# Performance work log

Hardware: AMD Instinct MI355X
Metric: run time of the kernel (lower is better)

## Reference

```python
import jax, jax.numpy as jnp
import numpy as np

B, T, D, H = 4, 1024, 1024, 16
DH = D // H
BETA = 0.9


def setup_inputs() -> dict:
    key = jax.random.key(0)
    ks = jax.random.split(key, 9)
    s = 1.0 / np.sqrt(D)
    return {
        "x": jax.random.normal(ks[0], (B, T, D), jnp.float32),
        "l3_memory": jax.random.normal(ks[1], (B, 1, D), jnp.float32),
        "wq": jax.random.normal(ks[2], (D, D), jnp.float32) * s,
        "wk": jax.random.normal(ks[3], (D, D), jnp.float32) * s,
        "wv": jax.random.normal(ks[4], (D, D), jnp.float32) * s,
        "wo": jax.random.normal(ks[5], (D, D), jnp.float32) * s,
        "rw1": jax.random.normal(ks[6], (D, D // 2), jnp.float32) * s,
        "rb1": jnp.zeros((D // 2,), jnp.float32),
        "rw2": jax.random.normal(ks[7], (D // 2, 3), jnp.float32) * (1.0 / np.sqrt(D // 2)),
        "rb2": jnp.zeros((3,), jnp.float32),
    }


def reference(x, l3_memory, wq, wk, wv, wo, rw1, rb1, rw2, rb2):
    b, t, d = x.shape
    dh = d // H

    def heads(y):  # [b,t,d] -> [b,h,t,dh]
        return y.reshape(b, t, H, dh).transpose(0, 2, 1, 3)

    q = x @ wq
    qh = heads(q)

    # L2: causal prefix EMA along time: y_t = beta*y_{t-1} + (1-beta)*x_t, y_{-1}=0
    def ema_step(c, xt):
        y = BETA * c + (1.0 - BETA) * xt
        return y, y
    _, l2 = jax.lax.scan(ema_step, jnp.zeros((b, d), x.dtype), jnp.swapaxes(x, 0, 1))
    l2 = jnp.swapaxes(l2, 0, 1)

    # L3: retrieval memory repeated to sequence length
    l3 = jnp.broadcast_to(l3_memory, (b, t, d))

    mask = jnp.tril(jnp.ones((t, t), bool))
    neg = jnp.finfo(x.dtype).min
    scale = 1.0 / np.sqrt(dh)

    def attend(mem):
        kh = heads(mem @ wk)
        vh = heads(mem @ wv)
        s = jnp.einsum('bhqd,bhkd->bhqk', qh, kh) * scale
        s = jnp.where(mask[None, None], s, neg)
        p = jax.nn.softmax(s, axis=-1)
        return jnp.einsum('bhqk,bhkd->bhqd', p, vh)

    # router over q tokens -> softmax mixture weights [b,t,3]
    hdn = jax.nn.gelu(q @ rw1 + rb1, approximate=False)
    lam = jax.nn.softmax(hdn @ rw2 + rb2, axis=-1)

    mixed = jnp.zeros((b, H, t, dh), x.dtype)
    for i, mem in enumerate((x, l2, l3)):
        mixed = mixed + lam[:, None, :, i:i + 1] * attend(mem)

    out = mixed.transpose(0, 2, 1, 3).reshape(b, t, d) @ wo
    return out, lam
```

## Files before the change

kernel.cpp:

```cpp
#include <hip/hip_runtime.h>
#include <hip/hip_bf16.h>
#include <math.h>


#define B_ 4
#define T_ 1024
#define D_ 1024
#define H_ 16
#define DH_ 64
#define M_ 4096

#define ECH 64
#define NCH 16

typedef __attribute__((ext_vector_type(8))) short bf16x8;
typedef __attribute__((ext_vector_type(4))) short s16x4;
typedef __attribute__((ext_vector_type(4))) float f32x4;
typedef __attribute__((ext_vector_type(4))) unsigned int u32x4;

__device__ inline short f2b(float f) {
  __hip_bfloat16 h = __float2bfloat16(f);
  return *reinterpret_cast<short*>(&h);
}

__device__ inline unsigned int pack2(float lo, float hi) {
  return ((unsigned int)(unsigned short)f2b(hi) << 16) |
         (unsigned int)(unsigned short)f2b(lo);
}

__device__ inline void gload_lds16(const short* g, short* l) {
  __builtin_amdgcn_global_load_lds(
      (const __attribute__((address_space(1))) unsigned int*)g,
      (__attribute__((address_space(3))) unsigned int*)l, 16, 0, 0);
}

__global__ __launch_bounds__(256) void ema_chunk_kernel(const float* __restrict__ x,
                                                        float* __restrict__ l2,
                                                        short* __restrict__ xb) {
  int idx = blockIdx.x * 256 + threadIdx.x;
  int d = idx & (D_ - 1);
  int ch = (idx >> 10) & (NCH - 1);
  int b = idx >> 14;
  const float* xp = x + (size_t)(b * T_ + ch * ECH) * D_ + d;
  float* yp = l2 + (size_t)(b * T_ + ch * ECH) * D_ + d;
  short* xbp = xb + (size_t)(b * T_ + ch * ECH) * D_ + d;
  float y = 0.f;
#pragma unroll 4
  for (int t = 0; t < ECH; ++t) {
    float xv = xp[t * D_];
    y = 0.9f * y + 0.1f * xv;
    yp[t * D_] = y;
    xbp[t * D_] = f2b(xv);
  }
}

__global__ __launch_bounds__(256) void ema_carry_kernel(const float* __restrict__ l2,
                                                        float* __restrict__ g) {
  int idx = blockIdx.x * 256 + threadIdx.x;
  int d = idx & (D_ - 1);
  int b = idx >> 10;
  const float b64 = 0.0011790184577739f;
  float G = 0.f;
  for (int ch = 0; ch < NCH; ++ch) {
    g[(size_t)(b * NCH + ch) * D_ + d] = G;
    float lf = l2[(size_t)(b * T_ + ch * ECH + ECH - 1) * D_ + d];
    G = lf + b64 * G;
  }
}

__global__ __launch_bounds__(256) void ema_fix_kernel(const float* __restrict__ l2,
                                                      const float* __restrict__ g,
                                                      short* __restrict__ l2b) {
  int idx = blockIdx.x * 256 + threadIdx.x;
  int d = idx & (D_ - 1);
  int t = (idx >> 10) & (T_ - 1);
  int b = idx >> 20;
  int ch = t >> 6;
  int off = t & (ECH - 1);
  float G = g[(size_t)(b * NCH + ch) * D_ + d];
  float p9 = exp2f((float)(off + 1) * -0.15200309344504997f);
  l2b[idx] = f2b(l2[idx] + p9 * G);
}

__global__ __launch_bounds__(256) void transpose_w_kernel(
    const float* __restrict__ w0, const float* __restrict__ w1,
    const float* __restrict__ w2, const float* __restrict__ w3,
    const float* __restrict__ w4,
    short* __restrict__ t0, short* __restrict__ t1, short* __restrict__ t2,
    short* __restrict__ t3, short* __restrict__ t4) {
  int z = blockIdx.z;
  const float* W = (z == 0) ? w0 : (z == 1) ? w1 : (z == 2) ? w2 : (z == 3) ? w3 : w4;
  short* Wt = (z == 0) ? t0 : (z == 1) ? t1 : (z == 2) ? t2 : (z == 3) ? t3 : t4;
  int cols = (z == 4) ? 512 : 1024;
  int c0 = blockIdx.x * 32, r0 = blockIdx.y * 32;
  if (c0 >= cols) return;
  __shared__ float tile[32][33];
  int tc = threadIdx.x & 31, tr8 = threadIdx.x >> 5;
#pragma unroll
  for (int i = 0; i < 4; ++i)
    tile[tr8 + i * 8][tc] = W[(size_t)(r0 + tr8 + i * 8) * cols + c0 + tc];
  __syncthreads();
#pragma unroll
  for (int i = 0; i < 4; ++i) {
    int rr = tr8 + i * 8;
    Wt[(size_t)(c0 + rr) * 1024 + r0 + tc] = f2b(tile[tc][rr]);
  }
}

template <int NB>
__global__ __launch_bounds__(256) void gemm_bt(const short* __restrict__ A, int lda,
                                               const short* __restrict__ Bt,
                                               float* __restrict__ Cf,
                                               short* __restrict__ Cb,
                                               int Ndim, int Kdim) {
  __shared__ short As[128 * 64];
  __shared__ short Bs[NB * 64];
  constexpr int NW = NB / 64;
  constexpr int NF = 4;
  constexpr int MF = (NW == 2) ? 4 : 2;
  int tid = threadIdx.x;
  int w = tid >> 6, l = tid & 63;
  int lg = l >> 4, ll = l & 15;
  int wr = (NW == 2) ? (w >> 1) : w;
  int wc = (NW == 2) ? (w & 1) : 0;
  int row0 = blockIdx.y * 128, col0 = blockIdx.x * NB;

  f32x4 acc[MF][NF];
#pragma unroll
  for (int m = 0; m < MF; ++m)
#pragma unroll
    for (int n = 0; n < NF; ++n) acc[m][n] = (f32x4){0.f, 0.f, 0.f, 0.f};

  for (int k0 = 0; k0 < Kdim; k0 += 64) {
    __syncthreads();
#pragma unroll
    for (int it = 0; it < 4; ++it) {
      int s = it * 256 + w * 64 + l;
      int r = s >> 3;
      int c = (s & 7) ^ (r & 7);
      gload_lds16(A + (size_t)(row0 + r) * lda + k0 + c * 8, &As[(it * 256 + w * 64) * 8]);
    }
#pragma unroll
    for (int it = 0; it < NB / 32; ++it) {
      int s = it * 256 + w * 64 + l;
      int r = s >> 3;
      int c = (s & 7) ^ (r & 7);
      gload_lds16(Bt + (size_t)(col0 + r) * Kdim + k0 + c * 8, &Bs[(it * 256 + w * 64) * 8]);
    }
    __syncthreads();
#pragma unroll
    for (int ks = 0; ks < 2; ++ks) {
      bf16x8 af[MF], bfr[NF];
#pragma unroll
      for (int m = 0; m < MF; ++m) {
        int r = wr * (MF * 16) + m * 16 + ll;
        af[m] = *(const bf16x8*)&As[r * 64 + (((ks * 4 + lg) ^ (r & 7)) << 3)];
      }
#pragma unroll
      for (int n = 0; n < NF; ++n) {
        int r = wc * 64 + n * 16 + ll;
        bfr[n] = *(const bf16x8*)&Bs[r * 64 + (((ks * 4 + lg) ^ (r & 7)) << 3)];
      }
#pragma unroll
      for (int m = 0; m < MF; ++m)
#pragma unroll
        for (int n = 0; n < NF; ++n)
          acc[m][n] = __builtin_amdgcn_mfma_f32_16x16x32_bf16(af[m], bfr[n], acc[m][n], 0, 0, 0);
    }
  }
#pragma unroll
  for (int m = 0; m < MF; ++m) {
    int gr = row0 + wr * (MF * 16) + m * 16 + lg * 4;
#pragma unroll
    for (int n = 0; n < NF; ++n) {
      int gc = col0 + wc * 64 + n * 16 + ll;
#pragma unroll
      for (int r = 0; r < 4; ++r) {
        float vv = acc[m][n][r];
        if (Cf) Cf[(size_t)(gr + r) * Ndim + gc] = vv;
        if (Cb) Cb[(size_t)(gr + r) * Ndim + gc] = f2b(vv);
      }
    }
  }
}

__global__ __launch_bounds__(256) void gemm_dual(const short* __restrict__ xb,
                                                 const short* __restrict__ l2b,
                                                 const short* __restrict__ wqkvT,
                                                 short* __restrict__ QKV,
                                                 short* __restrict__ KV2) {
  int lin = blockIdx.y * 40 + blockIdx.x;
  int lin2 = (lin & 7) * 160 + (lin >> 3);
  int bx = lin2 % 40;
  int by = lin2 / 40;

  const short* A;
  const short* Bt;
  short* Cb;
  int Ndim, col0;
  if (bx < 24) {
    A = xb; Bt = wqkvT; Cb = QKV; Ndim = 3072; col0 = bx * 128;
  } else {
    A = l2b; Bt = wqkvT + 1024 * 1024; Cb = KV2; Ndim = 2048; col0 = (bx - 24) * 128;
  }
  __shared__ short As[128 * 64];
  __shared__ short Bs[128 * 64];
  int tid = threadIdx.x;
  int w = tid >> 6, l = tid & 63;
  int lg = l >> 4, ll = l & 15;
  int wr = w >> 1, wc = w & 1;
  int row0 = by * 128;

  f32x4 acc[4][4];
#pragma unroll
  for (int m = 0; m < 4; ++m)
#pragma unroll
    for (int n = 0; n < 4; ++n) acc[m][n] = (f32x4){0.f, 0.f, 0.f, 0.f};

  for (int k0 = 0; k0 < 1024; k0 += 64) {
    __syncthreads();
#pragma unroll
    for (int it = 0; it < 4; ++it) {
      int s = it * 256 + w * 64 + l;
      int r = s >> 3;
      int c = (s & 7) ^ (r & 7);
      gload_lds16(A + (size_t)(row0 + r) * 1024 + k0 + c * 8, &As[(it * 256 + w * 64) * 8]);
      gload_lds16(Bt + (size_t)(col0 + r) * 1024 + k0 + c * 8, &Bs[(it * 256 + w * 64) * 8]);
    }
    __syncthreads();
#pragma unroll
    for (int ks = 0; ks < 2; ++ks) {
      bf16x8 af[4], bfr[4];
#pragma unroll
      for (int m = 0; m < 4; ++m) {
        int r = wr * 64 + m * 16 + ll;
        af[m] = *(const bf16x8*)&As[r * 64 + (((ks * 4 + lg) ^ (r & 7)) << 3)];
      }
#pragma unroll
      for (int n = 0; n < 4; ++n) {
        int r = wc * 64 + n * 16 + ll;
        bfr[n] = *(const bf16x8*)&Bs[r * 64 + (((ks * 4 + lg) ^ (r & 7)) << 3)];
      }
#pragma unroll
      for (int m = 0; m < 4; ++m)
#pragma unroll
        for (int n = 0; n < 4; ++n)
          acc[m][n] = __builtin_amdgcn_mfma_f32_16x16x32_bf16(af[m], bfr[n], acc[m][n], 0, 0, 0);
    }
  }
#pragma unroll
  for (int m = 0; m < 4; ++m) {
    int gr = row0 + wr * 64 + m * 16 + lg * 4;
#pragma unroll
    for (int n = 0; n < 4; ++n) {
      int gc = col0 + wc * 64 + n * 16 + ll;
#pragma unroll
      for (int r = 0; r < 4; ++r)
        Cb[(size_t)(gr + r) * Ndim + gc] = f2b(acc[m][n][r]);
    }
  }
}

__global__ __launch_bounds__(256) void v3_kernel(const float* __restrict__ l3,
                                                 const float* __restrict__ wv,
                                                 float* __restrict__ v3) {
  int idx = blockIdx.x * 256 + threadIdx.x;
  int b = idx >> 10;
  int col = idx & 1023;
  const float* xr = l3 + (size_t)b * D_;
  float acc = 0.f;
#pragma unroll 8
  for (int k = 0; k < D_; ++k) acc += xr[k] * wv[(size_t)k * D_ + col];
  v3[idx] = acc;
}

__global__ __launch_bounds__(256) void router_kernel(const float* __restrict__ hdnp,
                                                     const float* __restrict__ rb1,
                                                     const float* __restrict__ rw2,
                                                     const float* __restrict__ rb2,
                                                     float* __restrict__ lam) {
  int wave = (blockIdx.x * 256 + threadIdx.x) >> 6;
  int lane = threadIdx.x & 63;
  const float* hr = hdnp + (size_t)wave * 512;
  float s0 = 0.f, s1 = 0.f, s2 = 0.f;
#pragma unroll
  for (int u = 0; u < 8; ++u) {
    int hcol = u * 64 + lane;
    float vv = hr[hcol] + rb1[hcol];
    float gl = 0.5f * vv * (1.0f + erff(vv * 0.70710678118654752f));
    s0 += gl * rw2[hcol * 3 + 0];
    s1 += gl * rw2[hcol * 3 + 1];
    s2 += gl * rw2[hcol * 3 + 2];
  }
#pragma unroll
  for (int off = 32; off; off >>= 1) {
    s0 += __shfl_xor(s0, off);
    s1 += __shfl_xor(s1, off);
    s2 += __shfl_xor(s2, off);
  }
  if (lane == 0) {
    float a = s0 + rb2[0], bb = s1 + rb2[1], c = s2 + rb2[2];
    float m = fmaxf(fmaxf(a, bb), c);
    float e0 = expf(a - m), e1 = expf(bb - m), e2 = expf(c - m);
    float inv = 1.0f / (e0 + e1 + e2);
    lam[(size_t)wave * 3 + 0] = e0 * inv;
    lam[(size_t)wave * 3 + 1] = e1 * inv;
    lam[(size_t)wave * 3 + 2] = e2 * inv;
  }
}

__global__ __launch_bounds__(256) void attn_fused_kernel(
    const short* __restrict__ q, int ldq,
    const short* __restrict__ k1, const short* __restrict__ v1, int ld1,
    const short* __restrict__ k2, const short* __restrict__ v2, int ld2,
    const float* __restrict__ lam, const float* __restrict__ v3,
    short* __restrict__ mixedb) {
  __shared__ short Ks[2][64][64];
  __shared__ short Vt[2][64][64];

  int bid = blockIdx.x;
  int half = bid >> 9, p = bid & 511;
  int bh = p & 63;
  int j = p >> 6;
  int qb = half ? j : (15 - j);
  int b = bh >> 4, h = bh & 15;
  int q0 = qb * 64;
  int tid = threadIdx.x;
  int w = tid >> 6, l = tid & 63;
  int lg = l >> 4, ll = l & 15;

  int qw0 = q0 + w * 16;
  bf16x8 qf[2];
  {
    const short* qr = q + (size_t)(b * T_ + qw0 + ll) * ldq + h * DH_;
    qf[0] = *(const bf16x8*)&qr[lg * 8];
    qf[1] = *(const bf16x8*)&qr[32 + lg * 8];
  }

  float m_[2];
  f32x4 o[2][4];
  f32x4 ol[2];
#pragma unroll
  for (int s = 0; s < 2; ++s) {
    m_[s] = -1e30f;
#pragma unroll
    for (int db = 0; db < 4; ++db) o[s][db] = (f32x4){0.f, 0.f, 0.f, 0.f};
    ol[s] = (f32x4){0.f, 0.f, 0.f, 0.f};
  }

  bf16x8 ones;
#pragma unroll
  for (int jj = 0; jj < 8; ++jj) ones[jj] = (short)0x3F80;

  int se = ll + (((2 * lg) & 3) << 4);
  int so = ll + (((2 * lg + 1) & 3) << 4);
  bool hi = (lg >= 2);

  const float SC = 0.125f * 1.44269504f;
  int nt = qb + 1;
  for (int t64 = 0; t64 < nt; ++t64) {
    int key0 = t64 * 64;
    __syncthreads();
#pragma unroll
    for (int s = 0; s < 2; ++s) {
      const short* kp = s ? k2 : k1;
      const short* vp = s ? v2 : v1;
      int ld = s ? ld2 : ld1;
#pragma unroll
      for (int it = 0; it < 2; ++it) {
        int e = it * 256 + w * 64 + l;
        int r = e >> 3;
        int cs = (e & 7) ^ (r & 7);
        gload_lds16(kp + (size_t)(b * T_ + key0 + r) * ld + h * DH_ + cs * 8,
                    (short*)Ks[s] + (it * 256 + w * 64) * 8);
      }
      {
        int kp2 = tid >> 3, c8 = tid & 7;
        size_t gi = (size_t)(b * T_ + key0 + kp2 * 2) * ld + h * DH_ + c8 * 8;
        bf16x8 va = *(const bf16x8*)&vp[gi];
        bf16x8 vb = *(const bf16x8*)&vp[gi + ld];
        unsigned int* Vtd = (unsigned int*)Vt[s];
#pragma unroll
        for (int jj = 0; jj < 8; ++jj) {
          int dh = c8 * 8 + jj;
          int X = ((dh ^ (dh >> 3)) & 7) << 2;
          Vtd[dh * 32 + (kp2 ^ X)] =
              ((unsigned int)(unsigned short)va[jj]) |
              (((unsigned int)(unsigned short)vb[jj]) << 16);
        }
      }
    }
    __syncthreads();
    if (key0 > qw0 + 15) continue;

#pragma unroll
    for (int s = 0; s < 2; ++s) {
      f32x4 c[4];
#pragma unroll
      for (int kt = 0; kt < 4; ++kt) c[kt] = (f32x4){0.f, 0.f, 0.f, 0.f};
      __builtin_amdgcn_s_setprio(1);
#pragma unroll
      for (int kt = 0; kt < 4; ++kt) {
        int kr = kt * 16 + ll;
        bf16x8 kfa = *(const bf16x8*)&Ks[s][kr][((lg ^ (kr & 7)) << 3)];
        bf16x8 kfb = *(const bf16x8*)&Ks[s][kr][(((4 + lg) ^ (kr & 7)) << 3)];
        c[kt] = __builtin_amdgcn_mfma_f32_16x16x32_bf16(kfa, qf[0], c[kt], 0, 0, 0);
        c[kt] = __builtin_amdgcn_mfma_f32_16x16x32_bf16(kfb, qf[1], c[kt], 0, 0, 0);
      }
      __builtin_amdgcn_s_setprio(0);

      float sv[16];
      int row = qw0 + ll;
      if (key0 + 63 <= qw0) {
#pragma unroll
        for (int kt = 0; kt < 4; ++kt)
#pragma unroll
          for (int r = 0; r < 4; ++r) sv[kt * 4 + r] = c[kt][r] * SC;
      } else {
#pragma unroll
        for (int kt = 0; kt < 4; ++kt)
#pragma unroll
          for (int r = 0; r < 4; ++r) {
            float t = c[kt][r] * SC;
            sv[kt * 4 + r] = (key0 + kt * 16 + lg * 4 + r > row) ? -1e30f : t;
          }
      }

      float mx = sv[0];
#pragma unroll
      for (int i = 1; i < 16; ++i) mx = fmaxf(mx, sv[i]);
      mx = fmaxf(mx, __shfl_xor(mx, 16));
      mx = fmaxf(mx, __shfl_xor(mx, 32));

      if (__any(mx > m_[s] + 8.f)) {
        float nm = fmaxf(m_[s], mx);
        float al = exp2f(m_[s] - nm);
        m_[s] = nm;
        ol[s] *= al;
#pragma unroll
        for (int db = 0; db < 4; ++db) o[s][db] *= al;
      }

      unsigned int pk[4][2];
#pragma unroll
      for (int kt = 0; kt < 4; ++kt) {
        float p0 = exp2f(sv[kt * 4 + 0] - m_[s]);
        float p1 = exp2f(sv[kt * 4 + 1] - m_[s]);
        float p2 = exp2f(sv[kt * 4 + 2] - m_[s]);
        float p3 = exp2f(sv[kt * 4 + 3] - m_[s]);
        pk[kt][0] = pack2(p0, p1);
        pk[kt][1] = pack2(p2, p3);
      }

      const unsigned int* Vtd = (const unsigned int*)Vt[s];
#pragma unroll
      for (int ks = 0; ks < 2; ++ks) {
        unsigned int a0 = __shfl(pk[2 * ks][0], se), b0 = __shfl(pk[2 * ks + 1][0], se);
        unsigned int a1 = __shfl(pk[2 * ks][1], se), b1 = __shfl(pk[2 * ks + 1][1], se);
        unsigned int a2 = __shfl(pk[2 * ks][0], so), b2 = __shfl(pk[2 * ks + 1][0], so);
        unsigned int a3 = __shfl(pk[2 * ks][1], so), b3 = __shfl(pk[2 * ks + 1][1], so);
        u32x4 pd = {hi ? b0 : a0, hi ? b1 : a1, hi ? b2 : a2, hi ? b3 : a3};
        bf16x8 pf = *(bf16x8*)&pd;
        __builtin_amdgcn_s_setprio(1);
        ol[s] = __builtin_amdgcn_mfma_f32_16x16x32_bf16(ones, pf, ol[s], 0, 0, 0);
#pragma unroll
        for (int db = 0; db < 4; ++db) {
          int dh = db * 16 + ll;
          int X = ((dh ^ (dh >> 3)) & 7) << 2;
          bf16x8 vf = *(const bf16x8*)&Vtd[dh * 32 + ((ks * 16 + lg * 4) ^ X)];
          o[s][db] = __builtin_amdgcn_mfma_f32_16x16x32_bf16(vf, pf, o[s][db], 0, 0, 0);
        }
        __builtin_amdgcn_s_setprio(0);
      }
    }
  }

  int grow = qw0 + ll;
  const float* lr = lam + (size_t)(b * T_ + grow) * 3;
  float w0 = lr[0] / ol[0][0];
  float w1 = lr[1] / ol[1][0];
  float w2 = lr[2];
#pragma unroll
  for (int db = 0; db < 4; ++db) {
    s16x4 pkv;
#pragma unroll
    for (int r = 0; r < 4; ++r) {
      int dcol = h * DH_ + db * 16 + lg * 4 + r;
      float val = w0 * o[0][db][r] + w1 * o[1][db][r] + w2 * v3[(b << 10) + dcol];
      pkv[r] = f2b(val);
    }
    *(s16x4*)&mixedb[(size_t)(b * T_ + grow) * D_ + h * DH_ + db * 16 + lg * 4] = pkv;
  }
}

extern "C" void kernel_launch(void* const* d_in, const int* in_sizes, int n_in,
                              void* d_out, int out_size, void* d_ws, size_t ws_size,
                              hipStream_t stream) {
  const float* x = (const float*)d_in[0];
  const float* l3m = (const float*)d_in[1];
  const float* wq = (const float*)d_in[2];
  const float* wk = (const float*)d_in[3];
  const float* wv = (const float*)d_in[4];
  const float* wo = (const float*)d_in[5];
  const float* rw1 = (const float*)d_in[6];
  const float* rb1 = (const float*)d_in[7];
  const float* rw2 = (const float*)d_in[8];
  const float* rb2 = (const float*)d_in[9];

  float* out = (float*)d_out;
  float* lam = out + (size_t)M_ * D_;

  float* ws = (float*)d_ws;
  float* l2 = ws;
  short* QKV = (short*)ws;
  float* hdnp = ws + 6291456;
  float* v3 = ws + 8388608;
  float* gbuf = ws + 8392704;
  short* sb = (short*)(ws + 8458240);
  short* xb = sb;
  short* l2b = sb + 4194304;
  short* KV2 = sb + 8388608;
  short* mixedb = sb + 16777216;
  short* wqkvT = sb + 20971520;
  short* woT = sb + 24117248;
  short* rw1T = sb + 25165824;

  dim3 blk(256);

  transpose_w_kernel<<<dim3(32, 32, 5), blk, 0, stream>>>(
      wq, wk, wv, wo, rw1,
      wqkvT, wqkvT + 1024 * 1024, wqkvT + 2048 * 1024, woT, rw1T);

  ema_chunk_kernel<<<256, blk, 0, stream>>>(x, l2, xb);
  ema_carry_kernel<<<16, blk, 0, stream>>>(l2, gbuf);
  ema_fix_kernel<<<16384, blk, 0, stream>>>(l2, gbuf, l2b);

  gemm_dual<<<dim3(40, 32), blk, 0, stream>>>(xb, l2b, wqkvT, QKV, KV2);

  gemm_bt<64><<<dim3(8, 32), blk, 0, stream>>>(QKV, 3072, rw1T, hdnp, (short*)nullptr, 512, 1024);
  router_kernel<<<1024, blk, 0, stream>>>(hdnp, rb1, rw2, rb2, lam);

  v3_kernel<<<16, blk, 0, stream>>>(l3m, wv, v3);

  attn_fused_kernel<<<1024, blk, 0, stream>>>(QKV, 3072,
                                              QKV + 1024, QKV + 2048, 3072,
                                              KV2, KV2 + 1024, 2048,
                                              lam, v3, mixedb);

  gemm_bt<64><<<dim3(16, 32), blk, 0, stream>>>(mixedb, 1024, woT, out, (short*)nullptr, 1024, 1024);
}
```

Baseline: 258.4 us.

## Double-buffer K/V tiles across memory sources to overlap loads with MFMA compute

The attention loop is restructured so that each iteration handles one (key block, memory source) unit. The next unit's K tile (async global-to-LDS) and V registers are prefetched into the alternate LDS buffer while the current unit is computed. This is meant to hide global load latency behind the QK and PV MFMAs, at the cost of one barrier per unit instead of two per key block, with the same LDS footprint. The block-to-q-tile ordering is also flipped, which changes when the heavy causal blocks are scheduled.

```diff
diff --git a/kernel.cpp b/kernel.cpp
--- a/kernel.cpp
+++ b/kernel.cpp
@@ -322,7 +322,7 @@
   int half = bid >> 9, p = bid & 511;
   int bh = p & 63;
   int j = p >> 6;
-  int qb = half ? j : (15 - j);
+  int qb = half ? (15 - j) : j;
   int b = bh >> 4, h = bh & 15;
   int q0 = qb * 64;
   int tid = threadIdx.x;
@@ -356,45 +356,62 @@
   int so = ll + (((2 * lg + 1) & 3) << 4);
   bool hi = (lg >= 2);
 
+  int kp2 = tid >> 3, c8 = tid & 7;
   const float SC = 0.125f * 1.44269504f;
-  int nt = qb + 1;
-  for (int t64 = 0; t64 < nt; ++t64) {
-    int key0 = t64 * 64;
-    __syncthreads();
-#pragma unroll
-    for (int s = 0; s < 2; ++s) {
-      const short* kp = s ? k2 : k1;
-      const short* vp = s ? v2 : v1;
-      int ld = s ? ld2 : ld1;
+
+  int nu = (qb + 1) * 2;
+
+  {
+#pragma unroll
+    for (int it = 0; it < 2; ++it) {
+      int e = it * 256 + w * 64 + l;
+      int r = e >> 3;
+      int cs = (e & 7) ^ (r & 7);
+      gload_lds16(k1 + (size_t)(b * T_ + r) * ld1 + h * DH_ + cs * 8,
+                  (short*)Ks[0] + (it * 256 + w * 64) * 8);
+    }
+    size_t gi = (size_t)(b * T_ + kp2 * 2) * ld1 + h * DH_ + c8 * 8;
+    bf16x8 va = *(const bf16x8*)&v1[gi];
+    bf16x8 vb = *(const bf16x8*)&v1[gi + ld1];
+    unsigned int* Vtd = (unsigned int*)Vt[0];
+#pragma unroll
+    for (int jj = 0; jj < 8; ++jj) {
+      int dh = c8 * 8 + jj;
+      int X = ((dh ^ (dh >> 3)) & 7) << 2;
+      Vtd[dh * 32 + (kp2 ^ X)] =
+          ((unsigned int)(unsigned short)va[jj]) |
+          (((unsigned int)(unsigned short)vb[jj]) << 16);
+    }
+  }
+  __syncthreads();
+
+  for (int u = 0; u < nu; ++u) {
+    int buf = u & 1, nbuf = buf ^ 1;
+    int s = u & 1;
+    int key0 = (u >> 1) * 64;
+    bool have_next = (u + 1 < nu);
+
+    bf16x8 va, vb;
+    if (have_next) {
+      int ns = (u + 1) & 1;
+      int nkey0 = ((u + 1) >> 1) * 64;
+      const short* nkp = ns ? k2 : k1;
+      const short* nvp = ns ? v2 : v1;
+      int nld = ns ? ld2 : ld1;
 #pragma unroll
       for (int it = 0; it < 2; ++it) {
         int e = it * 256 + w * 64 + l;
         int r = e >> 3;
         int cs = (e & 7) ^ (r & 7);
-        gload_lds16(kp + (size_t)(b * T_ + key0 + r) * ld + h * DH_ + cs * 8,
-                    (short*)Ks[s] + (it * 256 + w * 64) * 8);
-      }
-      {
-        int kp2 = tid >> 3, c8 = tid & 7;
-        size_t gi = (size_t)(b * T_ + key0 + kp2 * 2) * ld + h * DH_ + c8 * 8;
-        bf16x8 va = *(const bf16x8*)&vp[gi];
-        bf16x8 vb = *(const bf16x8*)&vp[gi + ld];
-        unsigned int* Vtd = (unsigned int*)Vt[s];
-#pragma unroll
-        for (int jj = 0; jj < 8; ++jj) {
-          int dh = c8 * 8 + jj;
-          int X = ((dh ^ (dh >> 3)) & 7) << 2;
-          Vtd[dh * 32 + (kp2 ^ X)] =
-              ((unsigned int)(unsigned short)va[jj]) |
-              (((unsigned int)(unsigned short)vb[jj]) << 16);
-        }
-      }
-    }
-    __syncthreads();
-    if (key0 > qw0 + 15) continue;
-
-#pragma unroll
-    for (int s = 0; s < 2; ++s) {
+        gload_lds16(nkp + (size_t)(b * T_ + nkey0 + r) * nld + h * DH_ + cs * 8,
+                    (short*)Ks[nbuf] + (it * 256 + w * 64) * 8);
+      }
+      size_t gi = (size_t)(b * T_ + nkey0 + kp2 * 2) * nld + h * DH_ + c8 * 8;
+      va = *(const bf16x8*)&nvp[gi];
+      vb = *(const bf16x8*)&nvp[gi + nld];
+    }
+
+    if (key0 <= qw0 + 15) {
       f32x4 c[4];
 #pragma unroll
       for (int kt = 0; kt < 4; ++kt) c[kt] = (f32x4){0.f, 0.f, 0.f, 0.f};
@@ -402,8 +419,8 @@
 #pragma unroll
       for (int kt = 0; kt < 4; ++kt) {
         int kr = kt * 16 + ll;
-        bf16x8 kfa = *(const bf16x8*)&Ks[s][kr][((lg ^ (kr & 7)) << 3)];
-        bf16x8 kfb = *(const bf16x8*)&Ks[s][kr][(((4 + lg) ^ (kr & 7)) << 3)];
+        bf16x8 kfa = *(const bf16x8*)&Ks[buf][kr][((lg ^ (kr & 7)) << 3)];
+        bf16x8 kfb = *(const bf16x8*)&Ks[buf][kr][(((4 + lg) ^ (kr & 7)) << 3)];
         c[kt] = __builtin_amdgcn_mfma_f32_16x16x32_bf16(kfa, qf[0], c[kt], 0, 0, 0);
         c[kt] = __builtin_amdgcn_mfma_f32_16x16x32_bf16(kfb, qf[1], c[kt], 0, 0, 0);
       }
@@ -452,7 +469,7 @@
         pk[kt][1] = pack2(p2, p3);
       }
 
-      const unsigned int* Vtd = (const unsigned int*)Vt[s];
+      const unsigned int* Vtd = (const unsigned int*)Vt[buf];
 #pragma unroll
       for (int ks = 0; ks < 2; ++ks) {
         unsigned int a0 = __shfl(pk[2 * ks][0], se), b0 = __shfl(pk[2 * ks + 1][0], se);
@@ -473,6 +490,19 @@
         __builtin_amdgcn_s_setprio(0);
       }
     }
+
+    if (have_next) {
+      unsigned int* Vtd = (unsigned int*)Vt[nbuf];
+#pragma unroll
+      for (int jj = 0; jj < 8; ++jj) {
+        int dh = c8 * 8 + jj;
+        int X = ((dh ^ (dh >> 3)) & 7) << 2;
+        Vtd[dh * 32 + (kp2 ^ X)] =
+            ((unsigned int)(unsigned short)va[jj]) |
+            (((unsigned int)(unsigned short)vb[jj]) << 16);
+      }
+    }
+    __syncthreads();
   }
 
   int grow = qw0 + ll;
```

Result: slower. 278.5 us (+7.8%).
